# Performance work log

Measured on AMD Instinct MI355X. Metric: run time of the kernel, lower is better.

## Reference

```python
import jax, jax.numpy as jnp
import numpy as np

N_HEADS = 16
D_HEAD = 64
TAU = 30.0
NEG = -1e9


def setup_inputs() -> dict:
    key = jax.random.key(0)
    k1, k2, k3, k4 = jax.random.split(key, 4)
    B, L, D = 2, 2048, 1024
    scale = 1.0 / np.sqrt(D)
    return {
        "input": jax.random.normal(k1, (B, L, D), dtype=jnp.float32),
        "attention_mask": jnp.ones((B, L), dtype=jnp.int32),
        "W_Q": jax.random.normal(k2, (N_HEADS * D_HEAD, D), dtype=jnp.float32) * scale,
        "W_K": jax.random.normal(k3, (N_HEADS * D_HEAD, D), dtype=jnp.float32) * scale,
        "W_V": jax.random.normal(k4, (N_HEADS * D_HEAD, D), dtype=jnp.float32) * scale,
    }


def reference(input, attention_mask, W_Q, W_K, W_V):
    B, L, D = input.shape
    # fused QKV projection (F.linear: x @ W.T), split into heads: [B, H, L, Dh]
    def proj(W):
        return jnp.einsum('bld,ed->ble', input, W).reshape(B, L, N_HEADS, D_HEAD).transpose(0, 2, 1, 3)
    q, k, v = proj(W_Q), proj(W_K), proj(W_V)
    S = jnp.einsum('bhqd,bhkd->bhqk', q, k) / np.sqrt(D_HEAD)  # [B,H,L,L]
    S = TAU * jnp.tanh(S)
    causal = jnp.tril(jnp.ones((L, L), dtype=bool))            # True = keep
    keep = causal[None, None, :, :] & (attention_mask[:, None, None, :] != 0)
    S = jnp.where(keep, S, NEG)
    attn = jax.nn.softmax(S, axis=-1)
    out = jnp.einsum('bhqk,bhkd->bhqd', attn, v)
    return out.transpose(0, 2, 1, 3).reshape(B, L, N_HEADS * D_HEAD)
```

## Files before the change

### kernel.cpp

```cpp
#include <hip/hip_runtime.h>
#include <hip/hip_bf16.h>


typedef unsigned short u16;
typedef __bf16 bf16x8 __attribute__((ext_vector_type(8)));
typedef float f32x4 __attribute__((ext_vector_type(4)));

#define MFMA(a, b, c) __builtin_amdgcn_mfma_f32_16x16x32_bf16(a, b, c, 0, 0, 0)

__device__ __forceinline__ u16 bf16rne(float f) {
    unsigned int u = __float_as_uint(f);
    u += 0x7fffu + ((u >> 16) & 1u);
    return (u16)(u >> 16);
}
__device__ __forceinline__ float bf16f(u16 h) {
    return __uint_as_float(((unsigned int)h) << 16);
}
__device__ __forceinline__ void split1(float f, u16& hi, u16& lo) {
    hi = bf16rne(f);
    lo = bf16rne(f - bf16f(hi));
}
__device__ __forceinline__ unsigned int pk2(float a, float b) {
    __hip_bfloat162 t = __float22bfloat162_rn(float2{a, b});
    return *(unsigned int*)&t;
}

__device__ __forceinline__ void gl16(const u16* g, u16* l) {
    __builtin_amdgcn_global_load_lds(
        (const __attribute__((address_space(1))) unsigned int*)g,
        (__attribute__((address_space(3))) unsigned int*)l, 16, 0, 0);
}

__global__ __launch_bounds__(256) void presplit(
    const float* __restrict__ X, const float* __restrict__ Wq,
    const float* __restrict__ Wk, const float* __restrict__ Wv,
    u16* __restrict__ Xh, u16* __restrict__ Xl,
    u16* __restrict__ Wqh, u16* __restrict__ Wql,
    u16* __restrict__ Wkh, u16* __restrict__ Wkl,
    u16* __restrict__ Wvh)
{
    int i = blockIdx.x * 256 + threadIdx.x;
    const float* src; u16 *dh, *dl; int off;
    if (i < 1048576)      { src = X;  dh = Xh;  dl = Xl;      off = i; }
    else if (i < 1310720) { src = Wq; dh = Wqh; dl = Wql;     off = i - 1048576; }
    else if (i < 1572864) { src = Wk; dh = Wkh; dl = Wkl;     off = i - 1310720; }
    else                  { src = Wv; dh = Wvh; dl = nullptr; off = i - 1572864; }
    float4 v = ((const float4*)src)[off];
    ushort4 h, l;
    split1(v.x, h.x, l.x); split1(v.y, h.y, l.y);
    split1(v.z, h.z, l.z); split1(v.w, h.w, l.w);
    ((ushort4*)dh)[off] = h;
    if (dl) ((ushort4*)dl)[off] = l;
}

__global__ __launch_bounds__(256, 4) void qkv_gemm(
    const u16* __restrict__ Xh, const u16* __restrict__ Xl,
    const u16* __restrict__ Wqh, const u16* __restrict__ Wql,
    const u16* __restrict__ Wkh, const u16* __restrict__ Wkl,
    const u16* __restrict__ Wvh,
    u16* __restrict__ Qh, u16* __restrict__ Ql,
    u16* __restrict__ Kh, u16* __restrict__ Kl,
    u16* __restrict__ VT)
{
    __shared__ __align__(16) u16 S[16384];
    u16* const Xhs = &S[0];
    u16* const Xls = &S[4096];
    u16* const Whs = &S[8192];
    u16* const Wls = &S[12288];
    const int tid = threadIdx.x;
    const int wave = tid >> 6, lane = tid & 63, quad = lane >> 4, c16 = lane & 15;
    const int id = blockIdx.x;
    const int nb = (((id >> 3) % 3) << 3) | (id & 7);
    const int m0 = ((id >> 3) / 3) * 128;
    const int mat = nb >> 3;
    const int n0 = (nb & 7) * 128;
    const u16* Bh = (mat == 0) ? Wqh : ((mat == 1) ? Wkh : Wvh);
    const u16* Bl = (mat == 0) ? Wql : Wkl;
    const int nseg = (mat < 2) ? 3 : 1;
    const int wm = (wave >> 1) * 64, wn = (wave & 1) * 64;

    const int srow0 = wave * 32 + (lane >> 2), scol = (lane & 3) * 8;

    f32x4 acc[4][4];
#pragma unroll
    for (int i = 0; i < 4; i++)
#pragma unroll
        for (int j = 0; j < 4; j++) acc[i][j] = (f32x4){0.f, 0.f, 0.f, 0.f};

    for (int kt = 0; kt < 32; kt++) {
        const int kcol = kt * 32;
#pragma unroll
        for (int s = 0; s < 2; s++) {
            int row = srow0 + s * 16;
            size_t go = (size_t)row * 1024 + kcol + scol;
            int lo = row * 32 + scol;
            gl16(Xh + (size_t)m0 * 1024 + go, &Xhs[lo]);
            gl16(Bh + (size_t)n0 * 1024 + go, &Whs[lo]);
            if (nseg == 3) {
                gl16(Xl + (size_t)m0 * 1024 + go, &Xls[lo]);
                gl16(Bl + (size_t)n0 * 1024 + go, &Wls[lo]);
            }
        }
        __syncthreads();
        for (int seg = 0; seg < nseg; seg++) {
            const u16* ap = (seg < 2) ? Xhs : Xls;
            const u16* bp = (seg == 1) ? Wls : Whs;
            bf16x8 af[4], bfr[4];
#pragma unroll
            for (int mt = 0; mt < 4; mt++)
                af[mt] = *(const bf16x8*)&ap[(wm + mt * 16 + c16) * 32 + quad * 8];
#pragma unroll
            for (int nt = 0; nt < 4; nt++)
                bfr[nt] = *(const bf16x8*)&bp[(wn + nt * 16 + c16) * 32 + quad * 8];
#pragma unroll
            for (int mt = 0; mt < 4; mt++)
#pragma unroll
                for (int nt = 0; nt < 4; nt++)
                    acc[mt][nt] = MFMA(af[mt], bfr[nt], acc[mt][nt]);
        }
        __syncthreads();
    }

    if (mat == 2) {
        u16* const T2 = &S[wave * 4096];
        const int nglob = n0 + wn + lane;
        const int hh = nglob >> 6, dh = nglob & 63;
        const int bh64 = ((m0 >> 11) * 16 + hh) * 64 + dh;
        u16* const vrow = VT + (size_t)bh64 * 2048 + (m0 & 2047) + wm;
#pragma unroll
        for (int half = 0; half < 2; half++) {
#pragma unroll
            for (int mt2 = 0; mt2 < 2; mt2++) {
                int mt = half * 2 + mt2;
#pragma unroll
                for (int nt = 0; nt < 4; nt++) {
                    uint2 d;
                    d.x = pk2(acc[mt][nt][0], acc[mt][nt][1]);
                    d.y = pk2(acc[mt][nt][2], acc[mt][nt][3]);
                    *(uint2*)&T2[(nt * 16 + c16) * 40 + mt2 * 16 + quad * 4] = d;
                }
            }
#pragma unroll
            for (int c = 0; c < 4; c++) {
                uint4 d = *(const uint4*)&T2[lane * 40 + c * 8];
                *(uint4*)&vrow[half * 32 + c * 8] = d;
            }
        }
    } else {
        const float scale = (mat == 0) ? 0.125f : 1.f;
#pragma unroll
        for (int mt = 0; mt < 4; mt++) {
#pragma unroll
            for (int nt = 0; nt < 4; nt++) {
#pragma unroll
                for (int reg = 0; reg < 4; reg++) {
                    int mm = m0 + wm + mt * 16 + quad * 4 + reg;
                    int n = n0 + wn + nt * 16 + c16;
                    int b_ = mm >> 11, l = mm & 2047;
                    int h = n >> 6, dh = n & 63;
                    float v = acc[mt][nt][reg] * scale;
                    u16 hi, lo; split1(v, hi, lo);
                    int idx = ((b_ * 16 + h) * 2048 + l) * 64 + dh;
                    if (mat == 0) { Qh[idx] = hi; Ql[idx] = lo; }
                    else          { Kh[idx] = hi; Kl[idx] = lo; }
                }
            }
        }
    }
}

__global__ __launch_bounds__(256, 4) void attn(
    const u16* __restrict__ Qh, const u16* __restrict__ Ql,
    const u16* __restrict__ Kh, const u16* __restrict__ Kl,
    const u16* __restrict__ VT, const int* __restrict__ AM,
    u16* __restrict__ Op, float* __restrict__ Lp)
{
    __shared__ __align__(16) u16 Khs[2][4096];
    __shared__ __align__(16) u16 Kls[2][4096];
    __shared__ __align__(16) u16 Ps[4096];

    const int tid = threadIdx.x, wave = tid >> 6, lane = tid & 63;
    const int quad = lane >> 4, c16 = lane & 15;
    const int bh = blockIdx.x;
    const int pr = blockIdx.y;
    const int sp = blockIdx.z;
    const int b_ = bh >> 4;
    const size_t base = (size_t)bh * 2048 * 64;

    const int swsub[2] = { (wave * 2) >> 2, (wave * 2 + 1) >> 2 };
    const int swrow[2] = { ((wave * 2) & 3) * 16 + (lane >> 2), ((wave * 2 + 1) & 3) * 16 + (lane >> 2) };
    const int scol = (lane & 3) * 8;

    auto stageK = [&](int k0, int buf) {
        const u16* Kht = Kh + base + (size_t)k0 * 64;
        const u16* Klt = Kl + base + (size_t)k0 * 64;
#pragma unroll
        for (int s = 0; s < 2; s++) {
            int sub = swsub[s], row = swrow[s];
            int lo = sub * 2048 + row * 32 + scol;
            gl16(Kht + (size_t)row * 64 + sub * 32 + scol, &Khs[buf][lo]);
            gl16(Klt + (size_t)row * 64 + sub * 32 + scol, &Kls[buf][lo]);
        }
    };

    for (int tix = 0; tix < 2; ++tix) {
        const int qt = tix ? pr : 31 - pr;
        const int q0 = qt * 64;

        const size_t qrow = base + (size_t)(q0 + wave * 16 + c16) * 64 + quad * 8;
        bf16x8 qh0 = *(const bf16x8*)&Qh[qrow];
        bf16x8 qh1 = *(const bf16x8*)&Qh[qrow + 32];
        bf16x8 ql0 = *(const bf16x8*)&Ql[qrow];
        bf16x8 ql1 = *(const bf16x8*)&Ql[qrow + 32];

        float rsl[4] = {0.f, 0.f, 0.f, 0.f};
        f32x4 o[4];
#pragma unroll
        for (int r = 0; r < 4; r++) o[r] = (f32x4){0.f, 0.f, 0.f, 0.f};

        if (sp <= qt) {
            stageK(sp * 64, 0);
            int cur = 0;
            for (int kb = sp; kb <= qt; kb += 2) {
                const int k0 = kb * 64;
                __syncthreads();
                if (kb + 2 <= qt) stageK(k0 + 128, cur ^ 1);

                int mk[4];
#pragma unroll
                for (int nt = 0; nt < 4; nt++)
                    mk[nt] = AM[b_ * 2048 + k0 + nt * 16 + c16];
                bf16x8 vf[4][2];
#pragma unroll
                for (int dt = 0; dt < 4; dt++) {
                    const size_t vrow = (size_t)(bh * 64 + dt * 16 + c16) * 2048 + k0 + quad * 8;
                    vf[dt][0] = *(const bf16x8*)&VT[vrow];
                    vf[dt][1] = *(const bf16x8*)&VT[vrow + 32];
                }
                const bool interior = (kb < qt);

                float p[4][4];
#pragma unroll
                for (int nt = 0; nt < 4; nt++) {
                    bf16x8 kh0 = *(const bf16x8*)&Khs[cur][(nt * 16 + c16) * 32 + quad * 8];
                    bf16x8 kh1 = *(const bf16x8*)&Khs[cur][2048 + (nt * 16 + c16) * 32 + quad * 8];
                    bf16x8 kl0 = *(const bf16x8*)&Kls[cur][(nt * 16 + c16) * 32 + quad * 8];
                    bf16x8 kl1 = *(const bf16x8*)&Kls[cur][2048 + (nt * 16 + c16) * 32 + quad * 8];
                    f32x4 sa = (f32x4){0.f, 0.f, 0.f, 0.f};
                    sa = MFMA(qh0, kh0, sa);
                    sa = MFMA(qh1, kh1, sa);
                    sa = MFMA(ql0, kh0, sa);
                    sa = MFMA(ql1, kh1, sa);
                    sa = MFMA(qh0, kl0, sa);
                    sa = MFMA(qh1, kl1, sa);
                    const int key = k0 + nt * 16 + c16;
                    const bool mok = (mk[nt] != 0);
#pragma unroll
                    for (int reg = 0; reg < 4; reg++) {
                        int qg = q0 + wave * 16 + quad * 4 + reg;
                        float x = sa[reg];
                        float e1 = __expf(2.f * x);
                        float r  = __builtin_amdgcn_rcpf(e1 + 1.f);
                        float pv = __expf(-60.f * r);
                        bool keep = mok && (interior || key <= qg);
                        pv = keep ? pv : 0.f;
                        p[nt][reg] = pv;
                        rsl[reg] += pv;
                    }
                }

#pragma unroll
                for (int nt = 0; nt < 4; nt++) {
                    int kl_ = nt * 16 + c16, sub = kl_ >> 5, kc = kl_ & 31;
#pragma unroll
                    for (int reg = 0; reg < 4; reg++)
                        Ps[sub * 2048 + (wave * 16 + quad * 4 + reg) * 32 + kc] = bf16rne(p[nt][reg]);
                }
                bf16x8 p0 = *(const bf16x8*)&Ps[(wave * 16 + c16) * 32 + quad * 8];
                bf16x8 p1 = *(const bf16x8*)&Ps[2048 + (wave * 16 + c16) * 32 + quad * 8];
#pragma unroll
                for (int dt = 0; dt < 4; dt++) {
                    o[dt] = MFMA(p0, vf[dt][0], o[dt]);
                    o[dt] = MFMA(p1, vf[dt][1], o[dt]);
                }
                cur ^= 1;
            }
        }
        __syncthreads();

        const size_t obase = (((size_t)sp * 1024 + (size_t)bh * 32 + qt) * 4096);
        const size_t lbase = (((size_t)sp * 1024 + (size_t)bh * 32 + qt) * 64);
        float lsum[4];
#pragma unroll
        for (int reg = 0; reg < 4; reg++) {
            float v = rsl[reg];
#pragma unroll
            for (int off = 1; off < 16; off <<= 1)
                v += __shfl_xor(v, off);
            lsum[reg] = v;
        }
        if (c16 == 0) {
#pragma unroll
            for (int reg = 0; reg < 4; reg++)
                Lp[lbase + wave * 16 + quad * 4 + reg] = lsum[reg];
        }
#pragma unroll
        for (int dt = 0; dt < 4; dt++)
#pragma unroll
            for (int reg = 0; reg < 4; reg++) {
                int row = wave * 16 + quad * 4 + reg;
                int d = dt * 16 + c16;
                Op[obase + row * 64 + d] = bf16rne(o[dt][reg]);
            }
    }
}

__global__ __launch_bounds__(256) void combine(
    const u16* __restrict__ Op, const float* __restrict__ Lp,
    float* __restrict__ Out)
{
    const int i = blockIdx.x * 256 + threadIdx.x;
    const size_t lin = (size_t)i * 4;
    const int d  = (int)(lin & 1023);
    const int h  = d >> 6, dd = d & 63;
    const int l  = (int)((lin >> 10) & 2047);
    const int b  = (int)(lin >> 21);
    const int qt = l >> 6, row = l & 63;
    const int bh = b * 16 + h;
    const size_t o0 = (((size_t)bh * 32 + qt) * 4096) + row * 64 + dd;
    const size_t o1 = o0 + (size_t)1024 * 4096;
    const size_t l0 = (((size_t)bh * 32 + qt) * 64) + row;
    ushort4 pa = *(const ushort4*)&Op[o0];
    ushort4 pb = *(const ushort4*)&Op[o1];
    float inv = __builtin_amdgcn_rcpf(Lp[l0] + Lp[l0 + 65536]);
    float4 r;
    r.x = (bf16f(pa.x) + bf16f(pb.x)) * inv;
    r.y = (bf16f(pa.y) + bf16f(pb.y)) * inv;
    r.z = (bf16f(pa.z) + bf16f(pb.z)) * inv;
    r.w = (bf16f(pa.w) + bf16f(pb.w)) * inv;
    *(float4*)&Out[lin] = r;
}

extern "C" void kernel_launch(void* const* d_in, const int* in_sizes, int n_in,
                              void* d_out, int out_size, void* d_ws, size_t ws_size,
                              hipStream_t stream) {
    const float* X  = (const float*)d_in[0];
    const int*   AM = (const int*)d_in[1];
    const float* Wq = (const float*)d_in[2];
    const float* Wk = (const float*)d_in[3];
    const float* Wv = (const float*)d_in[4];
    float* out = (float*)d_out;

    const size_t NE = (size_t)2 * 16 * 2048 * 64;
    const size_t WN = (size_t)1024 * 1024;
    u16* Qh  = (u16*)d_ws;
    u16* Ql  = Qh + NE;
    u16* Kh  = Ql + NE;
    u16* Kl  = Kh + NE;
    u16* VT  = Kl + NE;
    u16* Xh  = VT + NE;
    u16* Xl  = Xh + NE;
    u16* Wqh = Xl + NE;
    u16* Wql = Wqh + WN;
    u16* Wkh = Wql + WN;
    u16* Wkl = Wkh + WN;
    u16* Wvh = Wkl + WN;
    u16*   Op = Xh;
    float* Lp = (float*)Wqh;

    presplit<<<7168, 256, 0, stream>>>(X, Wq, Wk, Wv, Xh, Xl, Wqh, Wql, Wkh, Wkl, Wvh);
    qkv_gemm<<<768, 256, 0, stream>>>(Xh, Xl, Wqh, Wql, Wkh, Wkl, Wvh,
                                      Qh, Ql, Kh, Kl, VT);
    attn<<<dim3(32, 16, 2), 256, 0, stream>>>(Qh, Ql, Kh, Kl, VT, AM, Op, Lp);
    combine<<<4096, 256, 0, stream>>>(Op, Lp, out);
}
```

Measured before the change: 237.2 us.

## Split attention KV loop three ways and drop low-K LDS staging for occupancy

The key dimension of the attention kernel is now split across three blocks instead of two, and the combine kernel sums three partial outputs and denominators. Low-precision K tiles are read directly from global memory instead of being staged in shared memory. This cuts LDS use and allows the launch bound to rise to 6 blocks per CU. V loads are moved next to the PV MFMAs to shorten register live ranges. The costs are more global/L2 traffic for Kl and V, a larger partial-output buffer, and extra combine work.

```diff
diff --git a/kernel.cpp b/kernel.cpp
--- a/kernel.cpp
+++ b/kernel.cpp
@@ -169,14 +169,13 @@
     }
 }
 
-__global__ __launch_bounds__(256, 4) void attn(
+__global__ __launch_bounds__(256, 6) void attn(
     const u16* __restrict__ Qh, const u16* __restrict__ Ql,
     const u16* __restrict__ Kh, const u16* __restrict__ Kl,
     const u16* __restrict__ VT, const int* __restrict__ AM,
     u16* __restrict__ Op, float* __restrict__ Lp)
 {
     __shared__ __align__(16) u16 Khs[2][4096];
-    __shared__ __align__(16) u16 Kls[2][4096];
     __shared__ __align__(16) u16 Ps[4096];
 
     const int tid = threadIdx.x, wave = tid >> 6, lane = tid & 63;
@@ -193,13 +192,11 @@
 
     auto stageK = [&](int k0, int buf) {
         const u16* Kht = Kh + base + (size_t)k0 * 64;
-        const u16* Klt = Kl + base + (size_t)k0 * 64;
 #pragma unroll
         for (int s = 0; s < 2; s++) {
             int sub = swsub[s], row = swrow[s];
-            int lo = sub * 2048 + row * 32 + scol;
-            gl16(Kht + (size_t)row * 64 + sub * 32 + scol, &Khs[buf][lo]);
-            gl16(Klt + (size_t)row * 64 + sub * 32 + scol, &Kls[buf][lo]);
+            gl16(Kht + (size_t)row * 64 + sub * 32 + scol,
+                 &Khs[buf][sub * 2048 + row * 32 + scol]);
         }
     };
 
@@ -221,31 +218,25 @@
         if (sp <= qt) {
             stageK(sp * 64, 0);
             int cur = 0;
-            for (int kb = sp; kb <= qt; kb += 2) {
+            for (int kb = sp; kb <= qt; kb += 3) {
                 const int k0 = kb * 64;
                 __syncthreads();
-                if (kb + 2 <= qt) stageK(k0 + 128, cur ^ 1);
+                if (kb + 3 <= qt) stageK(k0 + 192, cur ^ 1);
 
                 int mk[4];
 #pragma unroll
                 for (int nt = 0; nt < 4; nt++)
                     mk[nt] = AM[b_ * 2048 + k0 + nt * 16 + c16];
-                bf16x8 vf[4][2];
-#pragma unroll
-                for (int dt = 0; dt < 4; dt++) {
-                    const size_t vrow = (size_t)(bh * 64 + dt * 16 + c16) * 2048 + k0 + quad * 8;
-                    vf[dt][0] = *(const bf16x8*)&VT[vrow];
-                    vf[dt][1] = *(const bf16x8*)&VT[vrow + 32];
-                }
                 const bool interior = (kb < qt);
 
                 float p[4][4];
 #pragma unroll
                 for (int nt = 0; nt < 4; nt++) {
+                    const size_t krow = base + (size_t)(k0 + nt * 16 + c16) * 64 + quad * 8;
+                    bf16x8 kl0 = *(const bf16x8*)&Kl[krow];
+                    bf16x8 kl1 = *(const bf16x8*)&Kl[krow + 32];
                     bf16x8 kh0 = *(const bf16x8*)&Khs[cur][(nt * 16 + c16) * 32 + quad * 8];
                     bf16x8 kh1 = *(const bf16x8*)&Khs[cur][2048 + (nt * 16 + c16) * 32 + quad * 8];
-                    bf16x8 kl0 = *(const bf16x8*)&Kls[cur][(nt * 16 + c16) * 32 + quad * 8];
-                    bf16x8 kl1 = *(const bf16x8*)&Kls[cur][2048 + (nt * 16 + c16) * 32 + quad * 8];
                     f32x4 sa = (f32x4){0.f, 0.f, 0.f, 0.f};
                     sa = MFMA(qh0, kh0, sa);
                     sa = MFMA(qh1, kh1, sa);
@@ -278,10 +269,14 @@
                 }
                 bf16x8 p0 = *(const bf16x8*)&Ps[(wave * 16 + c16) * 32 + quad * 8];
                 bf16x8 p1 = *(const bf16x8*)&Ps[2048 + (wave * 16 + c16) * 32 + quad * 8];
+
 #pragma unroll
                 for (int dt = 0; dt < 4; dt++) {
-                    o[dt] = MFMA(p0, vf[dt][0], o[dt]);
-                    o[dt] = MFMA(p1, vf[dt][1], o[dt]);
+                    const size_t vrow = (size_t)(bh * 64 + dt * 16 + c16) * 2048 + k0 + quad * 8;
+                    bf16x8 v0 = *(const bf16x8*)&VT[vrow];
+                    bf16x8 v1 = *(const bf16x8*)&VT[vrow + 32];
+                    o[dt] = MFMA(p0, v0, o[dt]);
+                    o[dt] = MFMA(p1, v1, o[dt]);
                 }
                 cur ^= 1;
             }
@@ -328,16 +323,17 @@
     const int qt = l >> 6, row = l & 63;
     const int bh = b * 16 + h;
     const size_t o0 = (((size_t)bh * 32 + qt) * 4096) + row * 64 + dd;
-    const size_t o1 = o0 + (size_t)1024 * 4096;
     const size_t l0 = (((size_t)bh * 32 + qt) * 64) + row;
+    const size_t OS = (size_t)1024 * 4096;
     ushort4 pa = *(const ushort4*)&Op[o0];
-    ushort4 pb = *(const ushort4*)&Op[o1];
-    float inv = __builtin_amdgcn_rcpf(Lp[l0] + Lp[l0 + 65536]);
+    ushort4 pb = *(const ushort4*)&Op[o0 + OS];
+    ushort4 pc = *(const ushort4*)&Op[o0 + 2 * OS];
+    float inv = __builtin_amdgcn_rcpf(Lp[l0] + Lp[l0 + 65536] + Lp[l0 + 131072]);
     float4 r;
-    r.x = (bf16f(pa.x) + bf16f(pb.x)) * inv;
-    r.y = (bf16f(pa.y) + bf16f(pb.y)) * inv;
-    r.z = (bf16f(pa.z) + bf16f(pb.z)) * inv;
-    r.w = (bf16f(pa.w) + bf16f(pb.w)) * inv;
+    r.x = (bf16f(pa.x) + bf16f(pb.x) + bf16f(pc.x)) * inv;
+    r.y = (bf16f(pa.y) + bf16f(pb.y) + bf16f(pc.y)) * inv;
+    r.z = (bf16f(pa.z) + bf16f(pb.z) + bf16f(pc.z)) * inv;
+    r.w = (bf16f(pa.w) + bf16f(pb.w) + bf16f(pc.w)) * inv;
     *(float4*)&Out[lin] = r;
 }
 
@@ -366,11 +362,11 @@
     u16* Wkl = Wkh + WN;
     u16* Wvh = Wkl + WN;
     u16*   Op = Xh;
-    float* Lp = (float*)Wqh;
+    float* Lp = (float*)Wvh;
 
     presplit<<<7168, 256, 0, stream>>>(X, Wq, Wk, Wv, Xh, Xl, Wqh, Wql, Wkh, Wkl, Wvh);
     qkv_gemm<<<768, 256, 0, stream>>>(Xh, Xl, Wqh, Wql, Wkh, Wkl, Wvh,
                                       Qh, Ql, Kh, Kl, VT);
-    attn<<<dim3(32, 16, 2), 256, 0, stream>>>(Qh, Ql, Kh, Kl, VT, AM, Op, Lp);
+    attn<<<dim3(32, 16, 3), 256, 0, stream>>>(Qh, Ql, Kh, Kl, VT, AM, Op, Lp);
     combine<<<4096, 256, 0, stream>>>(Op, Lp, out);
 }
```

Measured after the change: 338.6 us. 42.7% more time.
